# Kernel tuning notes

Hardware: AMD Instinct MI355X
Metric: run time of the kernel (lower is better)

Reference implementation:

```python
import jax, jax.numpy as jnp
import numpy as np
import math

MUL = 16            # multiplicity of every irrep in Rs_in / Rs_out
NUM_EDGES = 20000
NUM_BASIS = 64
HIDDEN = 128
R_MAX = 3.0
# tensor-product paths (l_in, l_out, l_filter) from selection_rule_in_out_sh
PATHS = [(0, 0, 0), (0, 1, 1), (1, 0, 1), (1, 1, 0), (1, 1, 1), (1, 1, 2)]


def _real_w3j():
    """Real Wigner-3j tensors, axes [m_out, m_in, m_f]; l=1 in e3nn (y,z,x) order."""
    perm = [1, 2, 0]  # cartesian (x,y,z) -> e3nn l=1 component order (y,z,x)
    eye3 = np.eye(3)
    eps = np.zeros((3, 3, 3))
    for i, j, k in [(0, 1, 2), (1, 2, 0), (2, 0, 1)]:
        eps[i, j, k] = 1.0
        eps[i, k, j] = -1.0
    s2 = 1.0 / np.sqrt(2.0)
    # orthonormal symmetric-traceless basis matching l=2 SH order (xy, yz, 3z2-r2, zx, x2-y2)
    B = np.zeros((3, 3, 5))
    B[0, 1, 0] = B[1, 0, 0] = s2
    B[1, 2, 1] = B[2, 1, 1] = s2
    B[:, :, 2] = np.diag([-1.0, -1.0, 2.0]) / np.sqrt(6.0)
    B[2, 0, 3] = B[0, 2, 3] = s2
    B[0, 0, 4] = s2
    B[1, 1, 4] = -s2
    T112 = B[perm][:, perm] / np.sqrt(5.0)  # [m_out(l1), m_in(l1), m_f(l2)]
    w = {
        (0, 0, 0): np.ones((1, 1, 1)),
        (0, 1, 1): (eye3 / np.sqrt(3.0)).reshape(3, 1, 3),
        (1, 0, 1): (eye3 / np.sqrt(3.0)).reshape(1, 3, 3),
        (1, 1, 0): (eye3 / np.sqrt(3.0)).reshape(3, 3, 1),
        (1, 1, 1): eps / np.sqrt(6.0),  # Levi-Civita invariant under cyclic perm
        (1, 1, 2): T112,
    }
    return {k: jnp.asarray(v, jnp.float32) for k, v in w.items()}


W3J = _real_w3j()


def setup_inputs() -> dict:
    key = jax.random.key(0)
    ks = jax.random.split(key, 5)
    mul_dim = len(PATHS) * MUL * MUL  # 1536 radial channels
    return {
        "r": jax.random.normal(ks[0], (NUM_EDGES, 3), jnp.float32),
        "W1": jax.random.normal(ks[1], (NUM_BASIS, HIDDEN), jnp.float32) / math.sqrt(NUM_BASIS),
        "b1": jnp.zeros((HIDDEN,), jnp.float32),
        "W2": jax.random.normal(ks[2], (HIDDEN, mul_dim), jnp.float32) / math.sqrt(HIDDEN),
        "b2": jnp.zeros((mul_dim,), jnp.float32),
        "wl0": jax.random.normal(ks[3], (MUL, MUL), jnp.float32),
        "wl1": jax.random.normal(ks[4], (MUL, MUL), jnp.float32),
    }


def reference(r, W1, b1, W2, b2, wl0, wl1):
    E = r.shape[0]
    radii = jnp.linalg.norm(r, axis=1)
    mask = radii > 0.0  # r_eps = 0
    u = r / jnp.maximum(radii, 1e-12)[:, None]
    x, y, z = u[:, 0], u[:, 1], u[:, 2]
    # component-normalized real SH (already includes the sqrt(4*pi) factor)
    Y = {
        0: jnp.ones((E, 1), r.dtype),
        1: math.sqrt(3.0) * jnp.stack([y, z, x], -1),
        2: jnp.stack([
            math.sqrt(15.0) * x * y,
            math.sqrt(15.0) * y * z,
            (math.sqrt(5.0) / 2.0) * (3.0 * z * z - 1.0),
            math.sqrt(15.0) * z * x,
            (math.sqrt(15.0) / 2.0) * (x * x - y * y)], -1),
    }
    # radial MLP on gaussian basis embedding of |r|
    centers = jnp.linspace(0.0, R_MAX, NUM_BASIS).astype(r.dtype)
    width = R_MAX / NUM_BASIS
    basis = jnp.exp(-(((radii[:, None] - centers) / width) ** 2))
    h = jax.nn.silu(basis @ W1 + b1)
    Rw = (h @ W2 + b2).reshape(E, len(PATHS), MUL, MUL)  # [E, path, mul_out, mul_in]
    fan_in = {0: 2 * MUL, 1: 4 * MUL}  # sum of mul_in over paths into each l_out
    off = {0: 0, 1: MUL}               # flat offsets of the l-blocks (dim = 16 + 48)
    dim = 4 * MUL
    kernel1 = jnp.zeros((E, dim, dim), r.dtype)
    for p, (li, lo, lf) in enumerate(PATHS):
        norm = math.sqrt(2 * lo + 1) / math.sqrt(fan_in[lo])
        blk = norm * jnp.einsum('eoi,ef,abf->eoaib', Rw[:, p], Y[lf], W3J[(li, lo, lf)])
        do, di = MUL * (2 * lo + 1), MUL * (2 * li + 1)
        kernel1 = kernel1.at[:, off[lo]:off[lo] + do, off[li]:off[li] + di].add(
            blk.reshape(E, do, di))
    # KernelLinear: lmax=0 selection -> block-diagonal (W kron I_{2l+1}) / sqrt(mul_in)
    kernel2 = jnp.zeros((dim, dim), r.dtype)
    kernel2 = kernel2.at[:MUL, :MUL].set(wl0 / math.sqrt(MUL))
    kernel2 = kernel2.at[MUL:, MUL:].set(
        jnp.kron(wl1, jnp.eye(3, dtype=r.dtype)) / math.sqrt(MUL))
    return jnp.where(mask[:, None, None], kernel1, kernel2[None])
```

## Files before the change

### kernel.cpp

```cpp
#include <hip/hip_runtime.h>
#include <math.h>

#define E_TOTAL 20000
#define G 32
#define BLK 512
#define NB 64
#define HID 128
#define MULD 1536

typedef float f32x4 __attribute__((ext_vector_type(4)));
typedef short bf16x8 __attribute__((ext_vector_type(8)));

struct f3_t { float x, y, z; };

static __device__ __forceinline__ unsigned short f2bf(float f) {
    unsigned int u = __float_as_uint(f);
    unsigned int r = u + 0x7FFFu + ((u >> 16) & 1u);
    return (unsigned short)(r >> 16);
}
static __device__ __forceinline__ float bf2f(unsigned short h) {
    return __uint_as_float(((unsigned int)h) << 16);
}

__global__ __launch_bounds__(256) void prep_w2s(const float* __restrict__ W2,
                                                unsigned short* __restrict__ hi,
                                                unsigned short* __restrict__ lo) {
    const int i = blockIdx.x * 256 + threadIdx.x;
    const int j    = i & 7;
    const int lane = (i >> 3) & 63;
    const int kk   = (i >> 9) & 3;
    const int ntg  = i >> 11;
    const int k = kk*32 + (lane >> 4)*8 + j;
    const int n = ntg*16 + (lane & 15);
    const float f = W2[k * MULD + n];
    const unsigned short h = f2bf(f);
    hi[i] = h;
    lo[i] = f2bf(f - bf2f(h));
}

__global__ __launch_bounds__(BLK) void fused_tp_kernel(
    const float* __restrict__ r,
    const float* __restrict__ W1,
    const float* __restrict__ b1,
    const unsigned short* __restrict__ w2hs,
    const unsigned short* __restrict__ w2ls,
    const float* __restrict__ b2,
    const float* __restrict__ wl0,
    const float* __restrict__ wl1,
    float* __restrict__ out)
{
    __shared__ __align__(16) float s_h[G][132];
    __shared__ __align__(16) float s_basis[G][NB];
    __shared__ __align__(16) float s_b2[MULD];
    __shared__ float s_Y1[G][3];
    __shared__ float s_A1[G][9];
    __shared__ float s_A2[G][9];
    __shared__ float s_rad[G];
    __shared__ int   s_mask[G];

    const int t  = threadIdx.x;
    const int e0 = blockIdx.x * G;
    const int w  = t >> 6;
    const int l  = t & 63;
    const int lr = l & 15;
    const int lq = l >> 4;

    if (t < G) {
        const int e = e0 + t;
        float rx = r[e*3+0], ry = r[e*3+1], rz = r[e*3+2];
        float rad = sqrtf(rx*rx + ry*ry + rz*rz);
        s_rad[t]  = rad;
        s_mask[t] = (rad > 0.0f) ? 1 : 0;
        float inv = 1.0f / fmaxf(rad, 1e-12f);
        float x = rx*inv, y = ry*inv, z = rz*inv;

        const float SQ3  = 1.7320508075688772f;
        const float SQ15 = 3.872983346207417f;
        float Y10 = SQ3*y, Y11 = SQ3*z, Y12 = SQ3*x;
        s_Y1[t][0]=Y10; s_Y1[t][1]=Y11; s_Y1[t][2]=Y12;

        float Y20 = SQ15*x*y;
        float Y21 = SQ15*y*z;
        float Y22 = 1.118033988749895f*(3.f*z*z - 1.f);
        float Y23 = SQ15*z*x;
        float Y24 = 1.9364916731037085f*(x*x - y*y);

        const float n1  = 0.21650635094610965f;
        const float r6  = 0.4082482904638631f;
        const float cA1 = n1 * r6;
        s_A1[t][0] = 0.0f;      s_A1[t][1] =  cA1*Y12; s_A1[t][2] = -cA1*Y11;
        s_A1[t][3] = -cA1*Y12;  s_A1[t][4] = 0.0f;     s_A1[t][5] =  cA1*Y10;
        s_A1[t][6] =  cA1*Y11;  s_A1[t][7] = -cA1*Y10; s_A1[t][8] = 0.0f;

        const float s2 = 0.7071067811865476f;
        float M00 = -r6*Y22 + s2*Y24;
        float M01 =  s2*Y20;
        float M02 =  s2*Y23;
        float M11 = -r6*Y22 - s2*Y24;
        float M12 =  s2*Y21;
        float M22 =  2.0f*r6*Y22;
        const float c5 = n1 * 0.4472135954999579f;
        s_A2[t][0] = c5*M11; s_A2[t][1] = c5*M12; s_A2[t][2] = c5*M01;
        s_A2[t][3] = c5*M12; s_A2[t][4] = c5*M22; s_A2[t][5] = c5*M02;
        s_A2[t][6] = c5*M01; s_A2[t][7] = c5*M02; s_A2[t][8] = c5*M00;
    }
    __syncthreads();

    for (int idx = t; idx < G*NB; idx += BLK) {
        int g = idx >> 6, k = idx & 63;
        float rad = s_rad[g];
        float c = (3.0f * (float)k) * (1.0f/63.0f);
        float d = (rad - c) * (64.0f/3.0f);
        s_basis[g][k] = __expf(-d*d);
    }
    for (int idx = t; idx < MULD; idx += BLK) s_b2[idx] = b2[idx];
    __syncthreads();

    for (int idx = t; idx < G*32; idx += BLK) {
        const int g  = idx >> 5;
        const int c0 = (idx & 31) * 4;
        f32x4 acc = *reinterpret_cast<const f32x4*>(&b1[c0]);
#pragma unroll 8
        for (int k = 0; k < NB; ++k) {
            const f32x4 wv = *reinterpret_cast<const f32x4*>(&W1[k*HID + c0]);
            const float bv = s_basis[g][k];
            acc.x = fmaf(bv, wv.x, acc.x);
            acc.y = fmaf(bv, wv.y, acc.y);
            acc.z = fmaf(bv, wv.z, acc.z);
            acc.w = fmaf(bv, wv.w, acc.w);
        }
        f32x4 res;
        res.x = acc.x / (1.0f + __expf(-acc.x));
        res.y = acc.y / (1.0f + __expf(-acc.y));
        res.z = acc.z / (1.0f + __expf(-acc.z));
        res.w = acc.w / (1.0f + __expf(-acc.w));
        *reinterpret_cast<f32x4*>(&s_h[g][c0]) = res;
    }
    __syncthreads();

    bf16x8 ah0[4], al0[4], ah1[4], al1[4];
    {
        auto build = [&](const float* hrow, bf16x8* ah, bf16x8* al) {
#pragma unroll
            for (int kk = 0; kk < 4; ++kk) {
                f32x4 v0 = *reinterpret_cast<const f32x4*>(&hrow[kk*32 + lq*8]);
                f32x4 v1 = *reinterpret_cast<const f32x4*>(&hrow[kk*32 + lq*8 + 4]);
                float hv[8] = {v0.x, v0.y, v0.z, v0.w, v1.x, v1.y, v1.z, v1.w};
                bf16x8 h8, l8;
#pragma unroll
                for (int j = 0; j < 8; ++j) {
                    unsigned short hb = f2bf(hv[j]);
                    float rem = hv[j] - bf2f(hb);
                    h8[j] = (short)hb;
                    l8[j] = (short)f2bf(rem);
                }
                ah[kk] = h8; al[kk] = l8;
            }
        };
        build(&s_h[lr][0],      ah0, al0);
        build(&s_h[16 + lr][0], ah1, al1);
    }

    const float c00 = 0.17677669529663687f;
    const float cTR = 0.10206207261596577f;
    const float cBL = 0.125f;
    const float cD  = 0.125f;

    const bf16x8* ph = reinterpret_cast<const bf16x8*>(w2hs);
    const bf16x8* pl = reinterpret_cast<const bf16x8*>(w2ls);

    auto store_single = [&](f32x4 acc, int p, int nt, int eg) {
        if (p == 0) {
#pragma unroll
            for (int rr = 0; rr < 4; ++rr) {
                int e = eg*16 + lq*4 + rr;
                float v = c00 * acc[rr];
                __builtin_nontemporal_store(v, &out[(size_t)(e0+e)*4096 + nt*64 + lr]);
            }
        } else if (p == 1) {
#pragma unroll
            for (int rr = 0; rr < 4; ++rr) {
                int e = eg*16 + lq*4 + rr;
                float base = cBL * acc[rr];
#pragma unroll
                for (int a = 0; a < 3; ++a) {
                    float v = base * s_Y1[e][a];
                    __builtin_nontemporal_store(v, &out[(size_t)(e0+e)*4096 + (16 + nt*3 + a)*64 + lr]);
                }
            }
        } else {
#pragma unroll
            for (int rr = 0; rr < 4; ++rr) {
                int e = eg*16 + lq*4 + rr;
                float base = cTR * acc[rr];
                f3_t v = { base * s_Y1[e][0], base * s_Y1[e][1], base * s_Y1[e][2] };
                *reinterpret_cast<f3_t*>(&out[(size_t)(e0+e)*4096 + nt*64 + 16 + lr*3]) = v;
            }
        }
    };

    auto store_triple = [&](f32x4 a3, f32x4 a4, f32x4 a5, int o, int eg) {
#pragma unroll
        for (int rr = 0; rr < 4; ++rr) {
            int e = eg*16 + lq*4 + rr;
            const float* A1 = &s_A1[e][0];
            const float* A2 = &s_A2[e][0];
            float rv3 = cD * a3[rr], rv4 = a4[rr], rv5 = a5[rr];
            float* orow = &out[(size_t)(e0+e)*4096 + (16 + o*3)*64 + 16 + lr*3];
#pragma unroll
            for (int a = 0; a < 3; ++a) {
                f3_t v;
                float v0 = fmaf(rv4, A1[a*3+0], rv5 * A2[a*3+0]);
                float v1 = fmaf(rv4, A1[a*3+1], rv5 * A2[a*3+1]);
                float v2 = fmaf(rv4, A1[a*3+2], rv5 * A2[a*3+2]);
                if (a == 0) v0 += rv3;
                if (a == 1) v1 += rv3;
                if (a == 2) v2 += rv3;
                v.x = v0; v.y = v1; v.z = v2;
                *reinterpret_cast<f3_t*>(&orow[a*64]) = v;
            }
        }
    };

    const int items[12] = { w, w+8, w+16, w+24, w+32, w+40,
                            48+w, 64+w, 80+w, 56+w, 72+w, 88+w };

    bf16x8 B0h[4], B0l[4], B1h[4], B1l[4];
    auto loadB = [&](bf16x8* Bh, bf16x8* Bl, int ntg) {
#pragma unroll
        for (int kk = 0; kk < 4; ++kk) {
            Bh[kk] = ph[(ntg*4 + kk)*64 + l];
            Bl[kk] = pl[(ntg*4 + kk)*64 + l];
        }
    };
    auto mfma_item = [&](const bf16x8* Bh, const bf16x8* Bl, int ntg, f32x4& a0, f32x4& a1) {
        const float b2v = s_b2[ntg*16 + lr];
        a0 = f32x4{b2v, b2v, b2v, b2v};
        a1 = a0;
#pragma unroll
        for (int kk = 0; kk < 4; ++kk) {
            a0 = __builtin_amdgcn_mfma_f32_16x16x32_bf16(ah0[kk], Bh[kk], a0, 0, 0, 0);
            a1 = __builtin_amdgcn_mfma_f32_16x16x32_bf16(ah1[kk], Bh[kk], a1, 0, 0, 0);
            a0 = __builtin_amdgcn_mfma_f32_16x16x32_bf16(ah0[kk], Bl[kk], a0, 0, 0, 0);
            a1 = __builtin_amdgcn_mfma_f32_16x16x32_bf16(ah1[kk], Bl[kk], a1, 0, 0, 0);
            a0 = __builtin_amdgcn_mfma_f32_16x16x32_bf16(al0[kk], Bh[kk], a0, 0, 0, 0);
            a1 = __builtin_amdgcn_mfma_f32_16x16x32_bf16(al1[kk], Bh[kk], a1, 0, 0, 0);
        }
    };

    loadB(B0h, B0l, items[0]);
    f32x4 tri0[3], tri1[3];

#pragma unroll
    for (int i = 0; i < 12; ++i) {
        bf16x8* curH = (i & 1) ? B1h : B0h;
        bf16x8* curL = (i & 1) ? B1l : B0l;
        bf16x8* nxtH = (i & 1) ? B0h : B1h;
        bf16x8* nxtL = (i & 1) ? B0l : B1l;
        if (i < 11) loadB(nxtH, nxtL, items[i+1]);

        f32x4 a0, a1;
        mfma_item(curH, curL, items[i], a0, a1);

        if (i < 6) {
            const int p  = items[i] >> 4;
            const int nt = items[i] & 15;
            store_single(a0, p, nt, 0);
            store_single(a1, p, nt, 1);
        } else {
            const int ti = (i - 6) % 3;
            tri0[ti] = a0; tri1[ti] = a1;
            if (ti == 2) {
                const int o = (i < 9) ? w : (w + 8);
                store_triple(tri0[0], tri0[1], tri0[2], o, 0);
                store_triple(tri1[0], tri1[1], tri1[2], o, 1);
            }
        }
    }

    bool any = false;
#pragma unroll
    for (int e = 0; e < G; ++e) any |= (s_mask[e] == 0);
    if (any) {
        __syncthreads();
        for (int idx = t; idx < G*1024; idx += BLK) {
            int e = idx >> 10;
            if (s_mask[e]) continue;
            int q = idx & 1023;
            int row = q >> 4, col = (q & 15) * 4;
            float v[4];
#pragma unroll
            for (int j = 0; j < 4; ++j) {
                int cl = col + j;
                float val = 0.0f;
                if (row < 16 && cl < 16) {
                    val = wl0[row*16 + cl] * 0.25f;
                } else if (row >= 16 && cl >= 16) {
                    int o = (row-16)/3, aa = (row-16)%3;
                    int i2 = (cl-16)/3, bb = (cl-16)%3;
                    val = (aa == bb) ? wl1[o*16 + i2] * 0.25f : 0.0f;
                }
                v[j] = val;
            }
            f32x4 pack = {v[0], v[1], v[2], v[3]};
            __builtin_nontemporal_store(pack,
                reinterpret_cast<f32x4*>(&out[(size_t)(e0+e)*4096 + row*64 + col]));
        }
    }
}

extern "C" void kernel_launch(void* const* d_in, const int* in_sizes, int n_in,
                              void* d_out, int out_size, void* d_ws, size_t ws_size,
                              hipStream_t stream) {
    const float* r   = (const float*)d_in[0];
    const float* W1  = (const float*)d_in[1];
    const float* b1  = (const float*)d_in[2];
    const float* W2  = (const float*)d_in[3];
    const float* b2  = (const float*)d_in[4];
    const float* wl0 = (const float*)d_in[5];
    const float* wl1 = (const float*)d_in[6];
    float* out = (float*)d_out;

    unsigned short* w2hs = (unsigned short*)d_ws;
    unsigned short* w2ls = w2hs + (size_t)MULD * HID;

    prep_w2s<<<(MULD * HID) / 256, 256, 0, stream>>>(W2, w2hs, w2ls);

    const int nblocks = E_TOTAL / G;
    fused_tp_kernel<<<nblocks, BLK, 0, stream>>>(r, W1, b1, w2hs, w2ls, b2, wl0, wl1, out);
}
```

Measured before the change: 115.4 us.

## Halve edges per block to 16 with 256 threads, one MFMA row-tile per wave

Shrinks the per-block edge group from 32 to 16 and the block from 512 to 256 threads (4 waves). Each wave now computes one 16-edge row tile over twice as many W2 column items, instead of two row tiles sharing each loaded B fragment. This cuts A-fragment registers and doubles the number of blocks, which should help occupancy and load balance. In exchange each W2 B-fragment load is reused by only one MFMA chain, so W2 traffic per edge doubles.

```diff
diff --git a/kernel.cpp b/kernel.cpp
--- a/kernel.cpp
+++ b/kernel.cpp
@@ -2,8 +2,8 @@
 #include <math.h>
 
 #define E_TOTAL 20000
-#define G 32
-#define BLK 512
+#define G 16
+#define BLK 256
 #define NB 64
 #define HID 128
 #define MULD 1536
@@ -138,27 +138,24 @@
     }
     __syncthreads();
 
-    bf16x8 ah0[4], al0[4], ah1[4], al1[4];
+    bf16x8 ah[4], al[4];
     {
-        auto build = [&](const float* hrow, bf16x8* ah, bf16x8* al) {
-#pragma unroll
-            for (int kk = 0; kk < 4; ++kk) {
-                f32x4 v0 = *reinterpret_cast<const f32x4*>(&hrow[kk*32 + lq*8]);
-                f32x4 v1 = *reinterpret_cast<const f32x4*>(&hrow[kk*32 + lq*8 + 4]);
-                float hv[8] = {v0.x, v0.y, v0.z, v0.w, v1.x, v1.y, v1.z, v1.w};
-                bf16x8 h8, l8;
-#pragma unroll
-                for (int j = 0; j < 8; ++j) {
-                    unsigned short hb = f2bf(hv[j]);
-                    float rem = hv[j] - bf2f(hb);
-                    h8[j] = (short)hb;
-                    l8[j] = (short)f2bf(rem);
-                }
-                ah[kk] = h8; al[kk] = l8;
-            }
-        };
-        build(&s_h[lr][0],      ah0, al0);
-        build(&s_h[16 + lr][0], ah1, al1);
+        const float* hrow = &s_h[lr][0];
+#pragma unroll
+        for (int kk = 0; kk < 4; ++kk) {
+            f32x4 v0 = *reinterpret_cast<const f32x4*>(&hrow[kk*32 + lq*8]);
+            f32x4 v1 = *reinterpret_cast<const f32x4*>(&hrow[kk*32 + lq*8 + 4]);
+            float hv[8] = {v0.x, v0.y, v0.z, v0.w, v1.x, v1.y, v1.z, v1.w};
+            bf16x8 h8, l8;
+#pragma unroll
+            for (int j = 0; j < 8; ++j) {
+                unsigned short hb = f2bf(hv[j]);
+                float rem = hv[j] - bf2f(hb);
+                h8[j] = (short)hb;
+                l8[j] = (short)f2bf(rem);
+            }
+            ah[kk] = h8; al[kk] = l8;
+        }
     }
 
     const float c00 = 0.17677669529663687f;
@@ -169,18 +166,18 @@
     const bf16x8* ph = reinterpret_cast<const bf16x8*>(w2hs);
     const bf16x8* pl = reinterpret_cast<const bf16x8*>(w2ls);
 
-    auto store_single = [&](f32x4 acc, int p, int nt, int eg) {
+    auto store_single = [&](f32x4 acc, int p, int nt) {
         if (p == 0) {
 #pragma unroll
             for (int rr = 0; rr < 4; ++rr) {
-                int e = eg*16 + lq*4 + rr;
+                int e = lq*4 + rr;
                 float v = c00 * acc[rr];
                 __builtin_nontemporal_store(v, &out[(size_t)(e0+e)*4096 + nt*64 + lr]);
             }
         } else if (p == 1) {
 #pragma unroll
             for (int rr = 0; rr < 4; ++rr) {
-                int e = eg*16 + lq*4 + rr;
+                int e = lq*4 + rr;
                 float base = cBL * acc[rr];
 #pragma unroll
                 for (int a = 0; a < 3; ++a) {
@@ -191,7 +188,7 @@
         } else {
 #pragma unroll
             for (int rr = 0; rr < 4; ++rr) {
-                int e = eg*16 + lq*4 + rr;
+                int e = lq*4 + rr;
                 float base = cTR * acc[rr];
                 f3_t v = { base * s_Y1[e][0], base * s_Y1[e][1], base * s_Y1[e][2] };
                 *reinterpret_cast<f3_t*>(&out[(size_t)(e0+e)*4096 + nt*64 + 16 + lr*3]) = v;
@@ -199,10 +196,10 @@
         }
     };
 
-    auto store_triple = [&](f32x4 a3, f32x4 a4, f32x4 a5, int o, int eg) {
+    auto store_triple = [&](f32x4 a3, f32x4 a4, f32x4 a5, int o) {
 #pragma unroll
         for (int rr = 0; rr < 4; ++rr) {
-            int e = eg*16 + lq*4 + rr;
+            int e = lq*4 + rr;
             const float* A1 = &s_A1[e][0];
             const float* A2 = &s_A2[e][0];
             float rv3 = cD * a3[rr], rv4 = a4[rr], rv5 = a5[rr];
@@ -222,8 +219,12 @@
         }
     };
 
-    const int items[12] = { w, w+8, w+16, w+24, w+32, w+40,
-                            48+w, 64+w, 80+w, 56+w, 72+w, 88+w };
+    const int items[24] = {
+        w, w+4, w+8, w+12, w+16, w+20, w+24, w+28, w+32, w+36, w+40, w+44,
+        48+w,    64+w,    80+w,
+        48+w+4,  64+w+4,  80+w+4,
+        48+w+8,  64+w+8,  80+w+8,
+        48+w+12, 64+w+12, 80+w+12 };
 
     bf16x8 B0h[4], B0l[4], B1h[4], B1l[4];
     auto loadB = [&](bf16x8* Bh, bf16x8* Bl, int ntg) {
@@ -233,47 +234,41 @@
             Bl[kk] = pl[(ntg*4 + kk)*64 + l];
         }
     };
-    auto mfma_item = [&](const bf16x8* Bh, const bf16x8* Bl, int ntg, f32x4& a0, f32x4& a1) {
+    auto mfma_item = [&](const bf16x8* Bh, const bf16x8* Bl, int ntg) -> f32x4 {
         const float b2v = s_b2[ntg*16 + lr];
-        a0 = f32x4{b2v, b2v, b2v, b2v};
-        a1 = a0;
+        f32x4 a = f32x4{b2v, b2v, b2v, b2v};
 #pragma unroll
         for (int kk = 0; kk < 4; ++kk) {
-            a0 = __builtin_amdgcn_mfma_f32_16x16x32_bf16(ah0[kk], Bh[kk], a0, 0, 0, 0);
-            a1 = __builtin_amdgcn_mfma_f32_16x16x32_bf16(ah1[kk], Bh[kk], a1, 0, 0, 0);
-            a0 = __builtin_amdgcn_mfma_f32_16x16x32_bf16(ah0[kk], Bl[kk], a0, 0, 0, 0);
-            a1 = __builtin_amdgcn_mfma_f32_16x16x32_bf16(ah1[kk], Bl[kk], a1, 0, 0, 0);
-            a0 = __builtin_amdgcn_mfma_f32_16x16x32_bf16(al0[kk], Bh[kk], a0, 0, 0, 0);
-            a1 = __builtin_amdgcn_mfma_f32_16x16x32_bf16(al1[kk], Bh[kk], a1, 0, 0, 0);
-        }
+            a = __builtin_amdgcn_mfma_f32_16x16x32_bf16(ah[kk], Bh[kk], a, 0, 0, 0);
+            a = __builtin_amdgcn_mfma_f32_16x16x32_bf16(ah[kk], Bl[kk], a, 0, 0, 0);
+            a = __builtin_amdgcn_mfma_f32_16x16x32_bf16(al[kk], Bh[kk], a, 0, 0, 0);
+        }
+        return a;
     };
 
     loadB(B0h, B0l, items[0]);
-    f32x4 tri0[3], tri1[3];
-
-#pragma unroll
-    for (int i = 0; i < 12; ++i) {
+    f32x4 tri[3];
+
+#pragma unroll
+    for (int i = 0; i < 24; ++i) {
         bf16x8* curH = (i & 1) ? B1h : B0h;
         bf16x8* curL = (i & 1) ? B1l : B0l;
         bf16x8* nxtH = (i & 1) ? B0h : B1h;
         bf16x8* nxtL = (i & 1) ? B0l : B1l;
-        if (i < 11) loadB(nxtH, nxtL, items[i+1]);
-
-        f32x4 a0, a1;
-        mfma_item(curH, curL, items[i], a0, a1);
-
-        if (i < 6) {
+        if (i < 23) loadB(nxtH, nxtL, items[i+1]);
+
+        f32x4 a = mfma_item(curH, curL, items[i]);
+
+        if (i < 12) {
             const int p  = items[i] >> 4;
             const int nt = items[i] & 15;
-            store_single(a0, p, nt, 0);
-            store_single(a1, p, nt, 1);
+            store_single(a, p, nt);
         } else {
-            const int ti = (i - 6) % 3;
-            tri0[ti] = a0; tri1[ti] = a1;
+            const int ti = (i - 12) % 3;
+            tri[ti] = a;
             if (ti == 2) {
-                const int o = (i < 9) ? w : (w + 8);
-                store_triple(tri0[0], tri0[1], tri0[2], o, 0);
-                store_triple(tri1[0], tri1[1], tri1[2], o, 1);
+                const int o = w + ((i - 12) / 3) * 4;
+                store_triple(tri[0], tri[1], tri[2], o);
             }
         }
     }
```

Measured after the change: 98.27 us, median of 2. 1.17x faster.
